# Kernel tuning notes

Hardware: AMD Instinct MI355X
Metric: run time of the kernel (lower is better)

The kernel has to match this reference:

```python
import jax, jax.numpy as jnp
import numpy as np

H, D = 16, 64          # num_heads, head_dim
OUT = H * D            # out_dim = 1024
W1, W2 = 32, 32        # sliding windows
EPS_NORM = 1e-7
EPS_LN = 1e-5


def setup_inputs() -> dict:
    key = jax.random.key(0)
    ks = jax.random.split(key, 6)
    B, S, IN = 2, 2048, 1024
    x = jax.random.normal(ks[0], (B, S, IN), dtype=jnp.float32)
    scale = 0.02
    W_Q = jax.random.normal(ks[1], (IN, OUT), dtype=jnp.float32) * scale
    W_K = jax.random.normal(ks[2], (IN, OUT), dtype=jnp.float32) * scale
    W_V = jax.random.normal(ks[3], (IN, OUT), dtype=jnp.float32) * scale
    W_Kp = jax.random.normal(ks[4], (IN, OUT), dtype=jnp.float32) * scale
    W_O = jax.random.normal(ks[5], (OUT, OUT), dtype=jnp.float32) * scale
    ln_gamma = jnp.ones((OUT,), dtype=jnp.float32)
    ln_beta = jnp.zeros((OUT,), dtype=jnp.float32)
    return {"x": x, "W_Q": W_Q, "W_K": W_K, "W_V": W_V, "W_Kp": W_Kp,
            "W_O": W_O, "ln_gamma": ln_gamma, "ln_beta": ln_beta}


def _l2norm(t):
    return t / (jnp.linalg.norm(t, axis=-1, keepdims=True) + EPS_NORM)


def reference(x, W_Q, W_K, W_V, W_Kp, W_O, ln_gamma, ln_beta):
    B, S, _ = x.shape
    # projections -> (B, S, H, D)
    Q = _l2norm((x @ W_Q).reshape(B, S, H, D))
    K = _l2norm((x @ W_K).reshape(B, S, H, D))
    Kp = _l2norm((x @ W_Kp).reshape(B, S, H, D))
    V = (x @ W_V).reshape(B, S, H, D)
    # windowed keys/values (last w1/w2 positions, as in the PyTorch fallback)
    K_win = K[:, -W1:]
    Kp_win = Kp[:, -W2:]
    V_win = V[:, -W1:]
    Vp_win = V[:, -W2:]
    # triple product A_ijk = q.k.k' / sqrt(D) -> (B, S, H, w1, w2)
    A = jnp.einsum('bshd,bjhd,bkhd->bshjk', Q, K_win, Kp_win) / jnp.sqrt(jnp.float32(D))
    # causal window mask: allow j <= i + w1 - S and k <= i + w2 - S
    s_idx = jnp.arange(S)[:, None, None]
    j_idx = jnp.arange(W1)[None, :, None]
    k_idx = jnp.arange(W2)[None, None, :]
    mask = (j_idx > s_idx + (W1 - S)) | (k_idx > s_idx + (W2 - S))  # (S, w1, w2)
    neg_inf = jnp.float32(-jnp.inf)
    A = jnp.where(mask[None, :, None, :, :], neg_inf, A)
    # joint softmax over (j, k); fully-masked query rows produce zeros
    A_flat = A.reshape(B, S, H, W1 * W2)
    all_masked = jnp.all(A_flat == neg_inf, axis=-1, keepdims=True)
    A_safe = jnp.where(all_masked, 0.0, A_flat)
    P = jax.nn.softmax(A_safe, axis=-1)
    P = jnp.where(all_masked, 0.0, P).reshape(B, S, H, W1, W2)
    # value outer-product weighting (V' = V)
    Z = jnp.einsum('bshjk,bjhd,bkhd->bshd', P, V_win, Vp_win)
    out = Z.reshape(B, S, OUT) @ W_O
    out = out + x  # residual (shapes match)
    # LayerNorm
    mu = jnp.mean(out, axis=-1, keepdims=True)
    var = jnp.mean((out - mu) ** 2, axis=-1, keepdims=True)
    out = (out - mu) / jnp.sqrt(var + EPS_LN) * ln_gamma + ln_beta
    return out
```

## Files before the change

kernel.cpp:

```cpp
#include <hip/hip_runtime.h>
#include <math.h>


#define XS 68

#define YQ_OFF    0
#define YK_OFF    65536
#define YKP_OFF   131072
#define YV_OFF    196608
#define Z_OFF     262144
#define DELTA_OFF 327680
#define WS_FLOATS 393216

__global__ __launch_bounds__(256) void zero_ws(float4* __restrict__ ws) {
  ws[blockIdx.x * 256 + threadIdx.x] = make_float4(0.f, 0.f, 0.f, 0.f);
}

__global__ __launch_bounds__(256, 4) void proj_kernel(
    const float* __restrict__ x,
    const float* __restrict__ Wq, const float* __restrict__ Wk,
    const float* __restrict__ Wkp, const float* __restrict__ Wv,
    float* __restrict__ Y) {
  __shared__ float xs[64 * 65];
  const int tid = threadIdx.x;
  const int z    = blockIdx.x >> 4;
  const int col0 = (blockIdx.x & 15) * 64;
  const int k0   = blockIdx.y * 64;
  const float* __restrict__ W =
      (z == 0) ? Wq : ((z == 1) ? Wk : ((z == 2) ? Wkp : Wv));

  #pragma unroll
  for (int i = 0; i < 4; i++) {
    int e = i * 256 + tid;
    int r = e >> 4, q = e & 15;
    int b = r >> 5, t = r & 31;
    float4 v = *(const float4*)(x + ((b * 2048 + 2016 + t) * 1024 + k0 + q * 4));
    xs[(q * 4 + 0) * 65 + r] = v.x;
    xs[(q * 4 + 1) * 65 + r] = v.y;
    xs[(q * 4 + 2) * 65 + r] = v.z;
    xs[(q * 4 + 3) * 65 + r] = v.w;
  }
  __syncthreads();

  const int wave = __builtin_amdgcn_readfirstlane(tid >> 6);
  const int lane = tid & 63;
  const float* __restrict__ Wt = W + (size_t)k0 * 1024 + col0 + wave * 16;

  float acc[16];
  #pragma unroll
  for (int c = 0; c < 16; c++) acc[c] = 0.f;

  #pragma unroll 4
  for (int kk = 0; kk < 64; kk++) {
    float xv = xs[kk * 65 + lane];
    const float* __restrict__ wrow = Wt + kk * 1024;
    #pragma unroll
    for (int c = 0; c < 16; c++) acc[c] = fmaf(xv, wrow[c], acc[c]);
  }

  __syncthreads();
  #pragma unroll
  for (int c = 0; c < 16; c++) xs[lane * 65 + wave * 16 + c] = acc[c];
  __syncthreads();
  float* __restrict__ Yo = Y + z * 65536 + col0;
  #pragma unroll
  for (int i = 0; i < 16; i++) {
    int r = wave * 16 + i;
    atomicAdd(Yo + r * 1024 + lane, xs[r * 65 + lane]);
  }
}

__global__ __launch_bounds__(256) void attn_kernel(
    const float* __restrict__ Y, float* __restrict__ Zout) {
  __shared__ float Kn[32 * XS], Kp[32 * XS], Vs[32 * XS];
  __shared__ float Pt[4][32 * 33];
  __shared__ float qs[4][64];
  const int tid = threadIdx.x;
  const int wave = tid >> 6, lane = tid & 63;
  const int h = blockIdx.y, b = blockIdx.z;

  #pragma unroll
  for (int i = 0; i < 8; i++) {
    int e = i * 256 + tid;
    int row = e >> 6, d = e & 63;
    int src = (b * 32 + row) * 1024 + h * 64 + d;
    Kn[row * XS + d] = Y[YK_OFF + src];
    Kp[row * XS + d] = Y[YKP_OFF + src];
    Vs[row * XS + d] = Y[YV_OFF + src];
  }
  __syncthreads();

  for (int rr = 0; rr < 8; rr++) {
    int row = wave * 8 + rr;
    float kv = Kn[row * XS + lane];
    float s2 = kv * kv;
    #pragma unroll
    for (int off = 1; off < 64; off <<= 1) s2 += __shfl_xor(s2, off);
    Kn[row * XS + lane] = kv * (1.f / (sqrtf(s2) + 1e-7f));
    float pv = Kp[row * XS + lane];
    float p2 = pv * pv;
    #pragma unroll
    for (int off = 1; off < 64; off <<= 1) p2 += __shfl_xor(p2, off);
    Kp[row * XS + lane] = pv * (1.f / (sqrtf(p2) + 1e-7f));
  }
  __syncthreads();

  const int m = blockIdx.x * 4 + wave;
  const int r = b * 32 + m;

  float q = Y[YQ_OFF + r * 1024 + h * 64 + lane];
  float q2 = q * q;
  #pragma unroll
  for (int off = 1; off < 64; off <<= 1) q2 += __shfl_xor(q2, off);
  q *= (1.f / (sqrtf(q2) + 1e-7f));
  qs[wave][lane] = q;
  __builtin_amdgcn_wave_barrier();

  const int lj = lane >> 3, lk = lane & 7;
  float acc[4][4];
  #pragma unroll
  for (int a = 0; a < 4; a++)
    #pragma unroll
    for (int c = 0; c < 4; c++) acc[a][c] = 0.f;

  const float* qw = qs[wave];
  for (int dq = 0; dq < 16; dq++) {
    float4 q4 = *(const float4*)(qw + dq * 4);
    float4 t4[4], kp4[4];
    #pragma unroll
    for (int tj = 0; tj < 4; tj++) {
      float4 kv = *(const float4*)(Kn + (lj * 4 + tj) * XS + dq * 4);
      t4[tj].x = q4.x * kv.x; t4[tj].y = q4.y * kv.y;
      t4[tj].z = q4.z * kv.z; t4[tj].w = q4.w * kv.w;
    }
    #pragma unroll
    for (int tk = 0; tk < 4; tk++)
      kp4[tk] = *(const float4*)(Kp + (lk * 4 + tk) * XS + dq * 4);
    #pragma unroll
    for (int tj = 0; tj < 4; tj++)
      #pragma unroll
      for (int tk = 0; tk < 4; tk++)
        acc[tj][tk] += t4[tj].x * kp4[tk].x + t4[tj].y * kp4[tk].y
                     + t4[tj].z * kp4[tk].z + t4[tj].w * kp4[tk].w;
  }

  float amax = -1e30f;
  #pragma unroll
  for (int tj = 0; tj < 4; tj++)
    #pragma unroll
    for (int tk = 0; tk < 4; tk++) {
      int j = lj * 4 + tj, k = lk * 4 + tk;
      if (j <= m && k <= m) amax = fmaxf(amax, acc[tj][tk] * 0.125f);
    }
  #pragma unroll
  for (int off = 1; off < 64; off <<= 1) amax = fmaxf(amax, __shfl_xor(amax, off));

  float lsum = 0.f;
  float* ptw = Pt[wave];
  #pragma unroll
  for (int tj = 0; tj < 4; tj++)
    #pragma unroll
    for (int tk = 0; tk < 4; tk++) {
      int j = lj * 4 + tj, k = lk * 4 + tk;
      float e = 0.f;
      if (j <= m && k <= m) e = __expf(acc[tj][tk] * 0.125f - amax);
      lsum += e;
      ptw[k * 33 + j] = e;
    }
  #pragma unroll
  for (int off = 1; off < 64; off <<= 1) lsum += __shfl_xor(lsum, off);
  float inv = 1.f / lsum;
  __builtin_amdgcn_wave_barrier();

  float vreg[32];
  #pragma unroll
  for (int k = 0; k < 32; k++) vreg[k] = Vs[k * XS + lane];
  float zacc = 0.f;
  for (int k = 0; k <= m; k++) {
    float g = 0.f;
    #pragma unroll
    for (int j = 0; j < 32; j++) g += ptw[k * 33 + j] * vreg[j];
    zacc += g * vreg[k];
  }
  Zout[r * 1024 + h * 64 + lane] = zacc * inv;
}

__global__ __launch_bounds__(256, 4) void wo_kernel(
    const float* __restrict__ Zr, const float* __restrict__ Wo,
    float* __restrict__ delta) {
  __shared__ float xs[64 * 65];
  const int tid = threadIdx.x;
  const int col0 = blockIdx.x * 64;
  const int k0   = blockIdx.y * 32;

  #pragma unroll
  for (int i = 0; i < 2; i++) {
    int e = i * 256 + tid;
    int r = e >> 3, q = e & 7;
    float4 v = *(const float4*)(Zr + r * 1024 + k0 + q * 4);
    xs[(q * 4 + 0) * 65 + r] = v.x;
    xs[(q * 4 + 1) * 65 + r] = v.y;
    xs[(q * 4 + 2) * 65 + r] = v.z;
    xs[(q * 4 + 3) * 65 + r] = v.w;
  }
  __syncthreads();

  const int wave = __builtin_amdgcn_readfirstlane(tid >> 6);
  const int lane = tid & 63;
  const float* __restrict__ Wt = Wo + (size_t)k0 * 1024 + col0 + wave * 16;

  float acc[16];
  #pragma unroll
  for (int c = 0; c < 16; c++) acc[c] = 0.f;

  #pragma unroll 4
  for (int kk = 0; kk < 32; kk++) {
    float xv = xs[kk * 65 + lane];
    const float* __restrict__ wrow = Wt + kk * 1024;
    #pragma unroll
    for (int c = 0; c < 16; c++) acc[c] = fmaf(xv, wrow[c], acc[c]);
  }

  __syncthreads();
  #pragma unroll
  for (int c = 0; c < 16; c++) xs[lane * 65 + wave * 16 + c] = acc[c];
  __syncthreads();
  #pragma unroll
  for (int i = 0; i < 16; i++) {
    int r = wave * 16 + i;
    atomicAdd(delta + r * 1024 + col0 + lane, xs[r * 65 + lane]);
  }
}

__global__ __launch_bounds__(256, 4) void ln_kernel(
    const float4* __restrict__ x4, const float4* __restrict__ delta4,
    const float4* __restrict__ g4, const float4* __restrict__ b4,
    float4* __restrict__ out4) {
  const int tid = threadIdx.x;
  const int wave = tid >> 6, lane = tid & 63;
  const int row = blockIdx.x * 4 + wave;
  const int b = row >> 11, s = row & 2047;

  float4 v[4];
  #pragma unroll
  for (int i = 0; i < 4; i++) v[i] = x4[row * 256 + i * 64 + lane];
  if (s >= 2016) {
    int drow = b * 32 + (s - 2016);
    #pragma unroll
    for (int i = 0; i < 4; i++) {
      float4 d = delta4[drow * 256 + i * 64 + lane];
      v[i].x += d.x; v[i].y += d.y; v[i].z += d.z; v[i].w += d.w;
    }
  }
  float sum = 0.f, ss = 0.f;
  #pragma unroll
  for (int i = 0; i < 4; i++) {
    sum += v[i].x + v[i].y + v[i].z + v[i].w;
    ss  += v[i].x * v[i].x + v[i].y * v[i].y + v[i].z * v[i].z + v[i].w * v[i].w;
  }
  #pragma unroll
  for (int off = 1; off < 64; off <<= 1) {
    sum += __shfl_xor(sum, off);
    ss  += __shfl_xor(ss, off);
  }
  float mu   = sum * (1.f / 1024.f);
  float var  = ss * (1.f / 1024.f) - mu * mu;
  float rstd = rsqrtf(var + 1e-5f);

  #pragma unroll
  for (int i = 0; i < 4; i++) {
    float4 g = g4[i * 64 + lane];
    float4 be = b4[i * 64 + lane];
    float4 o;
    o.x = (v[i].x - mu) * rstd * g.x + be.x;
    o.y = (v[i].y - mu) * rstd * g.y + be.y;
    o.z = (v[i].z - mu) * rstd * g.z + be.z;
    o.w = (v[i].w - mu) * rstd * g.w + be.w;
    out4[row * 256 + i * 64 + lane] = o;
  }
}

extern "C" void kernel_launch(void* const* d_in, const int* in_sizes, int n_in,
                              void* d_out, int out_size, void* d_ws, size_t ws_size,
                              hipStream_t stream) {
  const float* x   = (const float*)d_in[0];
  const float* Wq  = (const float*)d_in[1];
  const float* Wk  = (const float*)d_in[2];
  const float* Wv  = (const float*)d_in[3];
  const float* Wkp = (const float*)d_in[4];
  const float* Wo  = (const float*)d_in[5];
  const float* gam = (const float*)d_in[6];
  const float* bet = (const float*)d_in[7];
  float* out = (float*)d_out;
  float* ws  = (float*)d_ws;

  hipLaunchKernelGGL(zero_ws, dim3(WS_FLOATS / 1024), dim3(256), 0, stream,
                     (float4*)ws);
  hipLaunchKernelGGL(proj_kernel, dim3(64, 16), dim3(256), 0, stream,
                     x, Wq, Wk, Wkp, Wv, ws);
  hipLaunchKernelGGL(attn_kernel, dim3(8, 16, 2), dim3(256), 0, stream,
                     ws, ws + Z_OFF);
  hipLaunchKernelGGL(wo_kernel, dim3(16, 32), dim3(256), 0, stream,
                     ws + Z_OFF, Wo, ws + DELTA_OFF);
  hipLaunchKernelGGL(ln_kernel, dim3(1024), dim3(256), 0, stream,
                     (const float4*)x, (const float4*)(ws + DELTA_OFF),
                     (const float4*)gam, (const float4*)bet, (float4*)out);
}
```

Before: 141.9 us.

## Split projection K-chunks, shrink attention blocks, swizzle LDS, use nontemporal LN stores

Result: slower. 159.1 us (+12.2%).

```diff
diff --git a/kernel.cpp b/kernel.cpp
--- a/kernel.cpp
+++ b/kernel.cpp
@@ -2,7 +2,7 @@
 #include <math.h>
 
 
-#define XS 68
+typedef float nfloat4 __attribute__((ext_vector_type(4)));
 
 #define YQ_OFF    0
 #define YK_OFF    65536
@@ -14,6 +14,10 @@
 
 __global__ __launch_bounds__(256) void zero_ws(float4* __restrict__ ws) {
   ws[blockIdx.x * 256 + threadIdx.x] = make_float4(0.f, 0.f, 0.f, 0.f);
+}
+
+__device__ __forceinline__ int sw_idx(int row, int d) {
+  return row * 64 + ((((d >> 2) + (row >> 2)) & 15) << 2) + (d & 3);
 }
 
 __global__ __launch_bounds__(256, 4) void proj_kernel(
@@ -25,14 +29,14 @@
   const int tid = threadIdx.x;
   const int z    = blockIdx.x >> 4;
   const int col0 = (blockIdx.x & 15) * 64;
-  const int k0   = blockIdx.y * 64;
+  const int k0   = blockIdx.y * 32;
   const float* __restrict__ W =
       (z == 0) ? Wq : ((z == 1) ? Wk : ((z == 2) ? Wkp : Wv));
 
   #pragma unroll
-  for (int i = 0; i < 4; i++) {
+  for (int i = 0; i < 2; i++) {
     int e = i * 256 + tid;
-    int r = e >> 4, q = e & 15;
+    int r = e >> 3, q = e & 7;
     int b = r >> 5, t = r & 31;
     float4 v = *(const float4*)(x + ((b * 2048 + 2016 + t) * 1024 + k0 + q * 4));
     xs[(q * 4 + 0) * 65 + r] = v.x;
@@ -51,7 +55,7 @@
   for (int c = 0; c < 16; c++) acc[c] = 0.f;
 
   #pragma unroll 4
-  for (int kk = 0; kk < 64; kk++) {
+  for (int kk = 0; kk < 32; kk++) {
     float xv = xs[kk * 65 + lane];
     const float* __restrict__ wrow = Wt + kk * 1024;
     #pragma unroll
@@ -70,51 +74,55 @@
   }
 }
 
-__global__ __launch_bounds__(256) void attn_kernel(
+__global__ __launch_bounds__(128) void attn_kernel(
     const float* __restrict__ Y, float* __restrict__ Zout) {
-  __shared__ float Kn[32 * XS], Kp[32 * XS], Vs[32 * XS];
-  __shared__ float Pt[4][32 * 33];
-  __shared__ float qs[4][64];
+  __shared__ float Kn[32 * 64], Kp[32 * 64];
+  __shared__ float Pt[2][32 * 36];
+  __shared__ float qs[2][64];
   const int tid = threadIdx.x;
   const int wave = tid >> 6, lane = tid & 63;
   const int h = blockIdx.y, b = blockIdx.z;
-
-  #pragma unroll
-  for (int i = 0; i < 8; i++) {
-    int e = i * 256 + tid;
+  const int m = blockIdx.x * 2 + wave;
+  const int r = b * 32 + m;
+
+  float vreg[32];
+  #pragma unroll
+  for (int k = 0; k < 32; k++)
+    vreg[k] = Y[YV_OFF + (b * 32 + k) * 1024 + h * 64 + lane];
+
+  float q = Y[YQ_OFF + r * 1024 + h * 64 + lane];
+
+  #pragma unroll
+  for (int i = 0; i < 16; i++) {
+    int e = i * 128 + tid;
     int row = e >> 6, d = e & 63;
     int src = (b * 32 + row) * 1024 + h * 64 + d;
-    Kn[row * XS + d] = Y[YK_OFF + src];
-    Kp[row * XS + d] = Y[YKP_OFF + src];
-    Vs[row * XS + d] = Y[YV_OFF + src];
-  }
-  __syncthreads();
-
-  for (int rr = 0; rr < 8; rr++) {
-    int row = wave * 8 + rr;
-    float kv = Kn[row * XS + lane];
+    Kn[sw_idx(row, d)] = Y[YK_OFF + src];
+    Kp[sw_idx(row, d)] = Y[YKP_OFF + src];
+  }
+  __syncthreads();
+
+  for (int rr = 0; rr < 16; rr++) {
+    int row = wave * 16 + rr;
+    int a = sw_idx(row, lane);
+    float kv = Kn[a];
     float s2 = kv * kv;
     #pragma unroll
     for (int off = 1; off < 64; off <<= 1) s2 += __shfl_xor(s2, off);
-    Kn[row * XS + lane] = kv * (1.f / (sqrtf(s2) + 1e-7f));
-    float pv = Kp[row * XS + lane];
+    Kn[a] = kv * (1.f / (sqrtf(s2) + 1e-7f));
+    float pv = Kp[a];
     float p2 = pv * pv;
     #pragma unroll
     for (int off = 1; off < 64; off <<= 1) p2 += __shfl_xor(p2, off);
-    Kp[row * XS + lane] = pv * (1.f / (sqrtf(p2) + 1e-7f));
-  }
-  __syncthreads();
-
-  const int m = blockIdx.x * 4 + wave;
-  const int r = b * 32 + m;
-
-  float q = Y[YQ_OFF + r * 1024 + h * 64 + lane];
+    Kp[a] = pv * (1.f / (sqrtf(p2) + 1e-7f));
+  }
+
   float q2 = q * q;
   #pragma unroll
   for (int off = 1; off < 64; off <<= 1) q2 += __shfl_xor(q2, off);
   q *= (1.f / (sqrtf(q2) + 1e-7f));
   qs[wave][lane] = q;
-  __builtin_amdgcn_wave_barrier();
+  __syncthreads();
 
   const int lj = lane >> 3, lk = lane & 7;
   float acc[4][4];
@@ -126,16 +134,18 @@
   const float* qw = qs[wave];
   for (int dq = 0; dq < 16; dq++) {
     float4 q4 = *(const float4*)(qw + dq * 4);
+    const int cj = (((dq + lj) & 15) << 2);
+    const int ck = (((dq + lk) & 15) << 2);
     float4 t4[4], kp4[4];
     #pragma unroll
     for (int tj = 0; tj < 4; tj++) {
-      float4 kv = *(const float4*)(Kn + (lj * 4 + tj) * XS + dq * 4);
+      float4 kv = *(const float4*)(Kn + (lj * 4 + tj) * 64 + cj);
       t4[tj].x = q4.x * kv.x; t4[tj].y = q4.y * kv.y;
       t4[tj].z = q4.z * kv.z; t4[tj].w = q4.w * kv.w;
     }
     #pragma unroll
     for (int tk = 0; tk < 4; tk++)
-      kp4[tk] = *(const float4*)(Kp + (lk * 4 + tk) * XS + dq * 4);
+      kp4[tk] = *(const float4*)(Kp + (lk * 4 + tk) * 64 + ck);
     #pragma unroll
     for (int tj = 0; tj < 4; tj++)
       #pragma unroll
@@ -158,29 +168,37 @@
   float lsum = 0.f;
   float* ptw = Pt[wave];
   #pragma unroll
-  for (int tj = 0; tj < 4; tj++)
-    #pragma unroll
-    for (int tk = 0; tk < 4; tk++) {
-      int j = lj * 4 + tj, k = lk * 4 + tk;
-      float e = 0.f;
-      if (j <= m && k <= m) e = __expf(acc[tj][tk] * 0.125f - amax);
-      lsum += e;
-      ptw[k * 33 + j] = e;
-    }
+  for (int tk = 0; tk < 4; tk++) {
+    int k = lk * 4 + tk;
+    float4 ev;
+    float* e = (float*)&ev;
+    #pragma unroll
+    for (int tj = 0; tj < 4; tj++) {
+      int j = lj * 4 + tj;
+      float xv = 0.f;
+      if (j <= m && k <= m) xv = __expf(acc[tj][tk] * 0.125f - amax);
+      e[tj] = xv;
+      lsum += xv;
+    }
+    *(float4*)(ptw + k * 36 + lj * 4) = ev;
+  }
   #pragma unroll
   for (int off = 1; off < 64; off <<= 1) lsum += __shfl_xor(lsum, off);
   float inv = 1.f / lsum;
   __builtin_amdgcn_wave_barrier();
 
-  float vreg[32];
-  #pragma unroll
-  for (int k = 0; k < 32; k++) vreg[k] = Vs[k * XS + lane];
   float zacc = 0.f;
   for (int k = 0; k <= m; k++) {
-    float g = 0.f;
-    #pragma unroll
-    for (int j = 0; j < 32; j++) g += ptw[k * 33 + j] * vreg[j];
-    zacc += g * vreg[k];
+    float g0 = 0.f, g1 = 0.f, g2 = 0.f, g3 = 0.f;
+    #pragma unroll
+    for (int jq = 0; jq < 8; jq++) {
+      float4 p = *(const float4*)(ptw + k * 36 + jq * 4);
+      g0 = fmaf(p.x, vreg[jq * 4 + 0], g0);
+      g1 = fmaf(p.y, vreg[jq * 4 + 1], g1);
+      g2 = fmaf(p.z, vreg[jq * 4 + 2], g2);
+      g3 = fmaf(p.w, vreg[jq * 4 + 3], g3);
+    }
+    zacc = fmaf((g0 + g1) + (g2 + g3), vreg[k], zacc);
   }
   Zout[r * 1024 + h * 64 + lane] = zacc * inv;
 }
@@ -271,12 +289,12 @@
   for (int i = 0; i < 4; i++) {
     float4 g = g4[i * 64 + lane];
     float4 be = b4[i * 64 + lane];
-    float4 o;
+    nfloat4 o;
     o.x = (v[i].x - mu) * rstd * g.x + be.x;
     o.y = (v[i].y - mu) * rstd * g.y + be.y;
     o.z = (v[i].z - mu) * rstd * g.z + be.z;
     o.w = (v[i].w - mu) * rstd * g.w + be.w;
-    out4[row * 256 + i * 64 + lane] = o;
+    __builtin_nontemporal_store(o, (nfloat4*)&out4[row * 256 + i * 64 + lane]);
   }
 }
 
@@ -296,9 +314,9 @@
 
   hipLaunchKernelGGL(zero_ws, dim3(WS_FLOATS / 1024), dim3(256), 0, stream,
                      (float4*)ws);
-  hipLaunchKernelGGL(proj_kernel, dim3(64, 16), dim3(256), 0, stream,
+  hipLaunchKernelGGL(proj_kernel, dim3(64, 32), dim3(256), 0, stream,
                      x, Wq, Wk, Wkp, Wv, ws);
-  hipLaunchKernelGGL(attn_kernel, dim3(8, 16, 2), dim3(256), 0, stream,
+  hipLaunchKernelGGL(attn_kernel, dim3(16, 16, 2), dim3(128), 0, stream,
                      ws, ws + Z_OFF);
   hipLaunchKernelGGL(wo_kernel, dim3(16, 32), dim3(256), 0, stream,
                      ws + Z_OFF, Wo, ws + DELTA_OFF);
```
